# Optimization experiments

Measured on AMD Instinct MI355X. Metric: run time of the kernel, lower is better.

Reference implementation:

```python
import jax, jax.numpy as jnp
import numpy as np

NEG_SLOPE = 0.2  # PyG GATConv default leaky_relu slope


def gat_conv(x, src, dst, num_nodes, W, att_src, att_dst, bias, heads, out_ch, concat):
    """PyG-style GATConv (eval mode, self-loops already included in src/dst).
    x: [N, in_ch]; src/dst: [E] int; W: [in_ch, heads*out_ch];
    att_src/att_dst: [heads, out_ch]; bias: [heads*out_ch] or [out_ch].
    """
    N = num_nodes
    h = (x @ W).reshape(N, heads, out_ch)                      # [N, H, C]
    a_src = jnp.einsum('nhc,hc->nh', h, att_src)               # [N, H]
    a_dst = jnp.einsum('nhc,hc->nh', h, att_dst)               # [N, H]
    e = jax.nn.leaky_relu(a_src[src] + a_dst[dst], NEG_SLOPE)  # [E, H]
    # segment softmax over incoming edges of each dst node
    m = jax.ops.segment_max(e, dst, num_segments=N)            # [N, H]
    m = jnp.where(jnp.isfinite(m), m, 0.0)
    w = jnp.exp(e - m[dst])                                    # [E, H]
    denom = jax.ops.segment_sum(w, dst, num_segments=N)        # [N, H]
    alpha = w / denom[dst]                                     # [E, H]
    msg = alpha[:, :, None] * h[src]                           # [E, H, C]
    out = jax.ops.segment_sum(msg, dst, num_segments=N)        # [N, H, C]
    if concat:
        out = out.reshape(N, heads * out_ch)
    else:
        out = out.mean(axis=1)
    return out + bias


def setup_inputs() -> dict:
    key = jax.random.key(0)
    ks = jax.random.split(key, 10)
    N, E, in_ch, hidden, heads = 50000, 800000, 128, 64, 4
    x = jax.random.normal(ks[0], (N, in_ch), dtype=jnp.float32)
    edge_index = jax.random.randint(ks[1], (2, E), 0, N, dtype=jnp.int64)
    s1 = float(np.sqrt(1.0 / in_ch))
    W1 = jax.random.normal(ks[2], (in_ch, heads * hidden), dtype=jnp.float32) * s1
    att_src1 = jax.random.normal(ks[3], (heads, hidden), dtype=jnp.float32) * 0.1
    att_dst1 = jax.random.normal(ks[4], (heads, hidden), dtype=jnp.float32) * 0.1
    bias1 = jnp.zeros((heads * hidden,), dtype=jnp.float32)
    s2 = float(np.sqrt(1.0 / (heads * hidden)))
    W2 = jax.random.normal(ks[5], (heads * hidden, 1), dtype=jnp.float32) * s2
    att_src2 = jax.random.normal(ks[6], (1, 1), dtype=jnp.float32) * 0.1
    att_dst2 = jax.random.normal(ks[7], (1, 1), dtype=jnp.float32) * 0.1
    bias2 = jnp.zeros((1,), dtype=jnp.float32)
    return {"x": x, "edge_index": edge_index, "W1": W1, "att_src1": att_src1,
            "att_dst1": att_dst1, "bias1": bias1, "W2": W2, "att_src2": att_src2,
            "att_dst2": att_dst2, "bias2": bias2}


def reference(x, edge_index, W1, att_src1, att_dst1, bias1, W2, att_src2, att_dst2, bias2):
    N = x.shape[0]
    hidden, heads = 64, 4
    loops = jnp.arange(N, dtype=edge_index.dtype)
    src = jnp.concatenate([edge_index[0], loops])  # PyG adds self-loops
    dst = jnp.concatenate([edge_index[1], loops])
    # eval mode -> dropout is identity
    h = gat_conv(x, src, dst, N, W1, att_src1, att_dst1, bias1, heads, hidden, True)
    h = jax.nn.elu(h)
    out = gat_conv(h, src, dst, N, W2, att_src2, att_dst2, bias2, 1, 1, False)
    return out.squeeze(-1)  # [N]
```

## Files before the change

### kernel.cpp

```cpp
#include <hip/hip_runtime.h>
#include <hip/hip_fp16.h>
#include <math.h>

#define INC 128
#define F1 256
#define HEADS 4
#define NEG_SLOPE 0.2f

typedef _Float16 f16x8 __attribute__((ext_vector_type(8)));
typedef float f32x4 __attribute__((ext_vector_type(4)));

__global__ __launch_bounds__(256) void prep_kernel(
    const float* __restrict__ W1, _Float16* __restrict__ W1T,
    const float* __restrict__ att_s, const float* __restrict__ att_d,
    float* __restrict__ w1s, float* __restrict__ w1d,
    const int* __restrict__ ei, int* __restrict__ deg, int* __restrict__ rank,
    int E, int Etot, int nw1t)
{
    int b = blockIdx.x;
    if (b < nw1t) {
        int i = b * 256 + threadIdx.x;
        int k = i >> 8;
        int c = i & 255;
        W1T[c * 128 + k] = (_Float16)W1[i];
    } else if (b < nw1t + ((Etot + 255) >> 8)) {
        int e = (b - nw1t) * 256 + threadIdx.x;
        if (e < Etot) {
            int d = (e < E) ? ei[E + e] : (e - E);
            rank[e] = atomicAdd(&deg[d], 1);
        }
    } else {
        #pragma unroll
        for (int rep = 0; rep < 2; ++rep) {
            int idx = threadIdx.x + rep * 256;
            int h = idx >> 7;
            int k = idx & 127;
            float ss = 0.f, sd = 0.f;
            for (int c = 0; c < 64; ++c) {
                float w = W1[k * F1 + h * 64 + c];
                ss += w * att_s[h * 64 + c];
                sd += w * att_d[h * 64 + c];
            }
            w1s[h * 128 + k] = ss;
            w1d[h * 128 + k] = sd;
        }
    }
}

__global__ __launch_bounds__(256) void scan1_kernel(
    const int* __restrict__ deg, int* __restrict__ incl,
    int* __restrict__ bsum, int N)
{
    __shared__ int tmp[256];
    int i = blockIdx.x * 256 + threadIdx.x;
    int v = (i < N) ? deg[i] : 0;
    tmp[threadIdx.x] = v;
    __syncthreads();
    for (int o = 1; o < 256; o <<= 1) {
        int add = (threadIdx.x >= o) ? tmp[threadIdx.x - o] : 0;
        __syncthreads();
        tmp[threadIdx.x] += add;
        __syncthreads();
    }
    if (i < N) incl[i] = tmp[threadIdx.x];
    if (threadIdx.x == 255) bsum[blockIdx.x] = tmp[255];
}

__global__ __launch_bounds__(256) void scan3_kernel(
    const int* __restrict__ deg, const int* __restrict__ incl,
    const int* __restrict__ bsum, int* __restrict__ off,
    int N, int Etot, int nb)
{
    __shared__ int tmp[256];
    const int bid = blockIdx.x;
    const int t = threadIdx.x;
    tmp[t] = (t < bid && t < nb) ? bsum[t] : 0;
    __syncthreads();
    #pragma unroll
    for (int o = 128; o > 0; o >>= 1) {
        if (t < o) tmp[t] += tmp[t + o];
        __syncthreads();
    }
    int pre = tmp[0];
    int i = bid * 256 + t;
    if (i < N) {
        off[i] = incl[i] - deg[i] + pre;
    } else if (i == N) {
        off[N] = Etot;
    }
}

__global__ __launch_bounds__(256) void mid_kernel(
    const int* __restrict__ ei, const int* __restrict__ rank,
    const int* __restrict__ off, int* __restrict__ esrc,
    const float* __restrict__ x, const float* __restrict__ w1s,
    const float* __restrict__ w1d, float* __restrict__ a_src,
    float* __restrict__ a_dst, unsigned* __restrict__ x_h,
    int N, int E, int Etot, int egrid)
{
    if ((int)blockIdx.x < egrid) {
        int e = blockIdx.x * 256 + threadIdx.x;
        if (e < Etot) {
            int s, d;
            if (e < E) { s = ei[e]; d = ei[E + e]; }
            else       { s = d = e - E; }
            esrc[off[d] + rank[e]] = s;
        }
        return;
    }
    int wave = threadIdx.x >> 6;
    int lane = threadIdx.x & 63;
    int n = (blockIdx.x - egrid) * 4 + wave;
    if (n >= N) return;
    float2 xv = *(const float2*)&x[(size_t)n * INC + lane * 2];
    __half2 xh = __floats2half2_rn(xv.x, xv.y);
    x_h[(size_t)n * 64 + lane] = *(unsigned*)&xh;
    float ps[4], pd[4];
    #pragma unroll
    for (int h = 0; h < 4; ++h) {
        float2 ws = *(const float2*)&w1s[h * 128 + lane * 2];
        float2 wd = *(const float2*)&w1d[h * 128 + lane * 2];
        ps[h] = xv.x * ws.x + xv.y * ws.y;
        pd[h] = xv.x * wd.x + xv.y * wd.y;
    }
    #pragma unroll
    for (int o = 32; o > 0; o >>= 1) {
        #pragma unroll
        for (int h = 0; h < 4; ++h) {
            ps[h] += __shfl_xor(ps[h], o);
            pd[h] += __shfl_xor(pd[h], o);
        }
    }
    if (lane == 0) {
        *(float4*)&a_src[n * HEADS] = make_float4(ps[0], ps[1], ps[2], ps[3]);
        *(float4*)&a_dst[n * HEADS] = make_float4(pd[0], pd[1], pd[2], pd[3]);
    }
}

__global__ __launch_bounds__(256) void aggx_kernel(
    const unsigned* __restrict__ x_h, const float* __restrict__ a_src,
    const float* __restrict__ a_dst, const int* __restrict__ off,
    const int* __restrict__ esrc, __half* __restrict__ agg, int N)
{
    __shared__ unsigned lalh[4][64][4];
    __shared__ int lsrc_s[4][64];

    const int wave = threadIdx.x >> 6;
    const int lane = threadIdx.x & 63;
    const int n = blockIdx.x * 4 + wave;
    if (n >= N) return;

    const int beg = off[n], end = off[n + 1];
    const int deg = end - beg;
    const float4* a_src4 = (const float4*)a_src;
    float4 ad4 = *(const float4*)&a_dst[n * HEADS];
    float ad[4] = {ad4.x, ad4.y, ad4.z, ad4.w};

    __half2 acc[4];
    #pragma unroll
    for (int h = 0; h < 4; ++h) acc[h] = __float2half2_rn(0.f);

    #define GATHER(CNT)                                                          \
    {                                                                            \
        int j = 0;                                                               \
        for (; j + 4 <= (CNT); j += 4) {                                         \
            int s0 = lsrc_s[wave][j + 0];                                        \
            int s1 = lsrc_s[wave][j + 1];                                        \
            int s2 = lsrc_s[wave][j + 2];                                        \
            int s3 = lsrc_s[wave][j + 3];                                        \
            unsigned v0 = x_h[(size_t)s0 * 64 + lane];                           \
            unsigned v1 = x_h[(size_t)s1 * 64 + lane];                           \
            unsigned v2 = x_h[(size_t)s2 * 64 + lane];                           \
            unsigned v3 = x_h[(size_t)s3 * 64 + lane];                           \
            uint4 a0 = *(uint4*)&lalh[wave][j + 0][0];                           \
            uint4 a1 = *(uint4*)&lalh[wave][j + 1][0];                           \
            uint4 a2 = *(uint4*)&lalh[wave][j + 2][0];                           \
            uint4 a3 = *(uint4*)&lalh[wave][j + 3][0];                           \
            __half2 h0 = *(__half2*)&v0, h1v = *(__half2*)&v1;                   \
            __half2 h2v = *(__half2*)&v2, h3 = *(__half2*)&v3;                   \
            acc[0] = __hfma2(*(__half2*)&a0.x, h0, acc[0]);                      \
            acc[1] = __hfma2(*(__half2*)&a0.y, h0, acc[1]);                      \
            acc[2] = __hfma2(*(__half2*)&a0.z, h0, acc[2]);                      \
            acc[3] = __hfma2(*(__half2*)&a0.w, h0, acc[3]);                      \
            acc[0] = __hfma2(*(__half2*)&a1.x, h1v, acc[0]);                     \
            acc[1] = __hfma2(*(__half2*)&a1.y, h1v, acc[1]);                     \
            acc[2] = __hfma2(*(__half2*)&a1.z, h1v, acc[2]);                     \
            acc[3] = __hfma2(*(__half2*)&a1.w, h1v, acc[3]);                     \
            acc[0] = __hfma2(*(__half2*)&a2.x, h2v, acc[0]);                     \
            acc[1] = __hfma2(*(__half2*)&a2.y, h2v, acc[1]);                     \
            acc[2] = __hfma2(*(__half2*)&a2.z, h2v, acc[2]);                     \
            acc[3] = __hfma2(*(__half2*)&a2.w, h2v, acc[3]);                     \
            acc[0] = __hfma2(*(__half2*)&a3.x, h3, acc[0]);                      \
            acc[1] = __hfma2(*(__half2*)&a3.y, h3, acc[1]);                      \
            acc[2] = __hfma2(*(__half2*)&a3.z, h3, acc[2]);                      \
            acc[3] = __hfma2(*(__half2*)&a3.w, h3, acc[3]);                      \
        }                                                                        \
        for (; j < (CNT); ++j) {                                                 \
            int s0 = lsrc_s[wave][j];                                            \
            unsigned v0 = x_h[(size_t)s0 * 64 + lane];                           \
            uint4 a0 = *(uint4*)&lalh[wave][j][0];                               \
            __half2 h0 = *(__half2*)&v0;                                         \
            acc[0] = __hfma2(*(__half2*)&a0.x, h0, acc[0]);                      \
            acc[1] = __hfma2(*(__half2*)&a0.y, h0, acc[1]);                      \
            acc[2] = __hfma2(*(__half2*)&a0.z, h0, acc[2]);                      \
            acc[3] = __hfma2(*(__half2*)&a0.w, h0, acc[3]);                      \
        }                                                                        \
    }

    if (deg <= 64) {
        int i = beg + lane;
        bool valid = i < end;
        int sN = esrc[valid ? i : beg];
        float4 a4 = a_src4[sN];
        float av[4] = {a4.x, a4.y, a4.z, a4.w};
        float ev[4];
        #pragma unroll
        for (int h = 0; h < 4; ++h) {
            float e = av[h] + ad[h];
            e = e > 0.f ? e : NEG_SLOPE * e;
            ev[h] = valid ? e : -1e30f;
        }
        float m[4] = {ev[0], ev[1], ev[2], ev[3]};
        #pragma unroll
        for (int o = 32; o > 0; o >>= 1) {
            #pragma unroll
            for (int h = 0; h < 4; ++h) m[h] = fmaxf(m[h], __shfl_xor(m[h], o));
        }
        float at[4];
        #pragma unroll
        for (int h = 0; h < 4; ++h) at[h] = valid ? __expf(ev[h] - m[h]) : 0.f;
        float s[4] = {at[0], at[1], at[2], at[3]};
        #pragma unroll
        for (int o = 32; o > 0; o >>= 1) {
            #pragma unroll
            for (int h = 0; h < 4; ++h) s[h] += __shfl_xor(s[h], o);
        }
        uint4 pack;
        __half2 t0 = __float2half2_rn(at[0] / s[0]);
        __half2 t1 = __float2half2_rn(at[1] / s[1]);
        __half2 t2 = __float2half2_rn(at[2] / s[2]);
        __half2 t3 = __float2half2_rn(at[3] / s[3]);
        pack.x = *(unsigned*)&t0; pack.y = *(unsigned*)&t1;
        pack.z = *(unsigned*)&t2; pack.w = *(unsigned*)&t3;
        *(uint4*)&lalh[wave][lane][0] = pack;
        lsrc_s[wave][lane] = sN;

        GATHER(deg);
    } else {
        float m[4] = {-1e30f, -1e30f, -1e30f, -1e30f};
        float s[4] = {0.f, 0.f, 0.f, 0.f};
        for (int i = beg + lane; i < end; i += 64) {
            int sN = esrc[i];
            float4 a4 = a_src4[sN];
            float av[4] = {a4.x, a4.y, a4.z, a4.w};
            #pragma unroll
            for (int h = 0; h < 4; ++h) {
                float e = av[h] + ad[h];
                e = e > 0.f ? e : NEG_SLOPE * e;
                float nm = fmaxf(m[h], e);
                s[h] = s[h] * __expf(m[h] - nm) + __expf(e - nm);
                m[h] = nm;
            }
        }
        #pragma unroll
        for (int o = 32; o > 0; o >>= 1) {
            #pragma unroll
            for (int h = 0; h < 4; ++h) {
                float om = __shfl_xor(m[h], o);
                float os = __shfl_xor(s[h], o);
                float nm = fmaxf(m[h], om);
                s[h] = s[h] * __expf(m[h] - nm) + os * __expf(om - nm);
                m[h] = nm;
            }
        }
        float inv[4];
        #pragma unroll
        for (int h = 0; h < 4; ++h) inv[h] = 1.f / s[h];

        for (int c0 = beg; c0 < end; c0 += 64) {
            int i = c0 + lane;
            if (i < end) {
                int sN = esrc[i];
                float4 a4 = a_src4[sN];
                float av[4] = {a4.x, a4.y, a4.z, a4.w};
                uint4 pack;
                #pragma unroll
                for (int h = 0; h < 4; ++h) {
                    float e = av[h] + ad[h];
                    e = e > 0.f ? e : NEG_SLOPE * e;
                    __half2 a2h = __float2half2_rn(__expf(e - m[h]) * inv[h]);
                    ((unsigned*)&pack)[h] = *(unsigned*)&a2h;
                }
                *(uint4*)&lalh[wave][lane][0] = pack;
                lsrc_s[wave][lane] = sN;
            }
            int cend = end - c0;
            if (cend > 64) cend = 64;
            GATHER(cend);
        }
    }
    #undef GATHER

    #pragma unroll
    for (int h = 0; h < 4; ++h)
        *(unsigned*)&agg[(size_t)n * 512 + h * 128 + lane * 2] = *(unsigned*)&acc[h];
}

__global__ __launch_bounds__(256, 4) void gemm2_kernel(
    const __half* __restrict__ agg, const _Float16* __restrict__ W1T,
    const float* __restrict__ bias1, const float* __restrict__ W2,
    float* __restrict__ z, int N)
{
    __shared__ __align__(16) _Float16 stg[32 * 520];
    __shared__ float zpart[2][32];

    const int tid = threadIdx.x;
    const int w = tid >> 6;
    const int lane = tid & 63;
    const int q = lane >> 4;
    const int c16 = lane & 15;
    const int row0 = blockIdx.x * 32;
    const int rg = w & 1;
    const int cg = w >> 1;

    #pragma unroll
    for (int it = 0; it < 8; ++it) {
        int flat = (tid + it * 256) * 8;
        int r = flat >> 9;
        int c = flat & 511;
        int row = row0 + r;
        uint4 v = (row < N) ? *(const uint4*)&agg[(size_t)row * 512 + c]
                            : make_uint4(0, 0, 0, 0);
        *(uint4*)&stg[r * 520 + c] = v;
    }
    __syncthreads();

    const int row_l = rg * 16 + c16;
    f16x8 af[2][4];
    #pragma unroll
    for (int hh = 0; hh < 2; ++hh) {
        int h = cg * 2 + hh;
        #pragma unroll
        for (int kc = 0; kc < 4; ++kc)
            af[hh][kc] = *(const f16x8*)&stg[row_l * 520 + h * 128 + kc * 32 + q * 8];
    }

    float pz[4] = {};
    #pragma unroll
    for (int hh = 0; hh < 2; ++hh) {
        #pragma unroll
        for (int t = 0; t < 4; ++t) {
            int col = cg * 128 + hh * 64 + t * 16 + c16;
            f32x4 acc = {0.f, 0.f, 0.f, 0.f};
            #pragma unroll
            for (int kc = 0; kc < 4; ++kc) {
                f16x8 b = *(const f16x8*)&W1T[(size_t)col * 128 + kc * 32 + q * 8];
                acc = __builtin_amdgcn_mfma_f32_16x16x32_f16(af[hh][kc], b, acc, 0, 0, 0);
            }
            float bv = bias1[col];
            float wv = W2[col];
            #pragma unroll
            for (int reg = 0; reg < 4; ++reg) {
                float o = acc[reg] + bv;
                o = o > 0.f ? o : __expf(o) - 1.f;
                pz[reg] = fmaf(o, wv, pz[reg]);
            }
        }
    }

    #pragma unroll
    for (int o = 8; o > 0; o >>= 1) {
        #pragma unroll
        for (int reg = 0; reg < 4; ++reg) pz[reg] += __shfl_xor(pz[reg], o);
    }
    if (c16 == 0) {
        #pragma unroll
        for (int reg = 0; reg < 4; ++reg)
            zpart[cg][rg * 16 + q * 4 + reg] = pz[reg];
    }
    __syncthreads();
    if (tid < 32) {
        int row = row0 + tid;
        if (row < N) z[row] = zpart[0][tid] + zpart[1][tid];
    }
}

__global__ __launch_bounds__(256) void agg2_kernel(
    const float* __restrict__ z, const int* __restrict__ off,
    const int* __restrict__ esrc, const float* __restrict__ att_s2,
    const float* __restrict__ att_d2, const float* __restrict__ bias2,
    float* __restrict__ out, int N)
{
    int wave = threadIdx.x >> 6;
    int lane = threadIdx.x & 63;
    int n = blockIdx.x * 4 + wave;
    if (n >= N) return;
    float as2 = att_s2[0], ad2 = att_d2[0];
    int beg = off[n], end = off[n + 1];
    int deg = end - beg;
    float dstterm = z[n] * ad2;

    if (deg <= 64) {
        int i = beg + lane;
        bool valid = i < end;
        int sN = esrc[valid ? i : beg];
        float zv = z[sN];
        float e = zv * as2 + dstterm;
        e = e > 0.f ? e : NEG_SLOPE * e;
        float ev = valid ? e : -1e30f;
        float m = ev;
        #pragma unroll
        for (int o = 32; o > 0; o >>= 1) m = fmaxf(m, __shfl_xor(m, o));
        float at = valid ? __expf(ev - m) : 0.f;
        float s = at, wv = at * zv;
        #pragma unroll
        for (int o = 32; o > 0; o >>= 1) {
            s += __shfl_xor(s, o);
            wv += __shfl_xor(wv, o);
        }
        if (lane == 0) out[n] = wv / s + bias2[0];
    } else {
        float m = -1e30f, s = 0.f, wv = 0.f;
        for (int i = beg + lane; i < end; i += 64) {
            int sN = esrc[i];
            float zv = z[sN];
            float e = zv * as2 + dstterm;
            e = e > 0.f ? e : NEG_SLOPE * e;
            float nm = fmaxf(m, e);
            float c0 = __expf(m - nm), c1 = __expf(e - nm);
            s = s * c0 + c1;
            wv = wv * c0 + c1 * zv;
            m = nm;
        }
        #pragma unroll
        for (int o = 32; o > 0; o >>= 1) {
            float om = __shfl_xor(m, o), os = __shfl_xor(s, o), ow = __shfl_xor(wv, o);
            float nm = fmaxf(m, om);
            float c0 = __expf(m - nm), c1 = __expf(om - nm);
            s = s * c0 + os * c1;
            wv = wv * c0 + ow * c1;
            m = nm;
        }
        if (lane == 0) out[n] = wv / s + bias2[0];
    }
}

extern "C" void kernel_launch(void* const* d_in, const int* in_sizes, int n_in,
                              void* d_out, int out_size, void* d_ws, size_t ws_size,
                              hipStream_t stream)
{
    const float* x        = (const float*)d_in[0];
    const int*   ei       = (const int*)d_in[1];
    const float* W1       = (const float*)d_in[2];
    const float* att_src1 = (const float*)d_in[3];
    const float* att_dst1 = (const float*)d_in[4];
    const float* bias1    = (const float*)d_in[5];
    const float* W2       = (const float*)d_in[6];
    const float* att_src2 = (const float*)d_in[7];
    const float* att_dst2 = (const float*)d_in[8];
    const float* bias2    = (const float*)d_in[9];
    float* out = (float*)d_out;

    int N = in_sizes[0] / INC;
    int E = in_sizes[1] / 2;
    int Etot = E + N;

    char* p = (char*)d_ws;
    auto alloc = [&](size_t bytes) {
        void* r = (void*)p;
        p += (bytes + 255) & ~(size_t)255;
        return r;
    };
    unsigned* x_h   = (unsigned*)alloc((size_t)N * 64 * 4);
    __half* agg     = (__half*)alloc((size_t)N * 512 * 2);
    _Float16* W1T   = (_Float16*)alloc((size_t)INC * F1 * 2);
    float* w1s    = (float*)alloc(4 * 128 * 4);
    float* w1d    = (float*)alloc(4 * 128 * 4);
    float* a_src1 = (float*)alloc((size_t)N * HEADS * 4);
    float* a_dst1 = (float*)alloc((size_t)N * HEADS * 4);
    float* z      = (float*)alloc((size_t)N * 4);
    int* deg    = (int*)alloc((size_t)N * 4);
    int* incl   = (int*)alloc((size_t)N * 4);
    int* off    = (int*)alloc((size_t)(N + 1) * 4);
    int* rank   = (int*)alloc((size_t)Etot * 4);
    int* bsum   = (int*)alloc(1024);
    int* esrc   = (int*)alloc((size_t)Etot * 4);

    hipMemsetAsync(deg, 0, (size_t)N * 4, stream);

    int nw1t = INC * F1 / 256;
    int egrid = (Etot + 255) / 256;
    prep_kernel<<<nw1t + egrid + 1, 256, 0, stream>>>(
        W1, W1T, att_src1, att_dst1, w1s, w1d, ei, deg, rank, E, Etot, nw1t);

    int nb = (N + 255) / 256;
    scan1_kernel<<<nb, 256, 0, stream>>>(deg, incl, bsum, N);

    int nb1 = (N + 1 + 255) / 256;
    scan3_kernel<<<nb1, 256, 0, stream>>>(deg, incl, bsum, off, N, Etot, nb);

    int nlog = (N + 3) / 4;
    mid_kernel<<<egrid + nlog, 256, 0, stream>>>(
        ei, rank, off, esrc, x, w1s, w1d, a_src1, a_dst1, x_h, N, E, Etot, egrid);

    int ngrid1 = (N + 3) / 4;
    aggx_kernel<<<ngrid1, 256, 0, stream>>>(x_h, a_src1, a_dst1, off, esrc, agg, N);

    int ng2 = (N + 31) / 32;
    gemm2_kernel<<<ng2, 256, 0, stream>>>(agg, W1T, bias1, W2, z, N);

    int ngrid2 = (N + 3) / 4;
    agg2_kernel<<<ngrid2, 256, 0, stream>>>(z, off, esrc, att_src2, att_dst2, bias2, out, N);
}
```

Measured before the change: 181.5 us.

## Fuse layer-1 aggregation with the second GEMM and ELU projection

The layer-1 aggregation kernel now stages its per-node fp16 aggregated features in shared memory, then runs the W1 MFMA product, bias, ELU and the dot product with W2 in the same block to produce z directly. This removes the separate gemm2 kernel and the round trip of the N×512 fp16 intermediate through global memory. In exchange each 4-node block re-reads all of W1T from cache, uses only 4 of 16 MFMA rows, and adds block-wide barriers that tie together waves whose nodes have uneven degrees.

```diff
diff --git a/kernel.cpp b/kernel.cpp
--- a/kernel.cpp
+++ b/kernel.cpp
@@ -9,6 +9,12 @@
 
 typedef _Float16 f16x8 __attribute__((ext_vector_type(8)));
 typedef float f32x4 __attribute__((ext_vector_type(4)));
+
+static __device__ __forceinline__ f16x8 f16x8_zero() {
+    f16x8 v = {(_Float16)0, (_Float16)0, (_Float16)0, (_Float16)0,
+               (_Float16)0, (_Float16)0, (_Float16)0, (_Float16)0};
+    return v;
+}
 
 __global__ __launch_bounds__(256) void prep_kernel(
     const float* __restrict__ W1, _Float16* __restrict__ W1T,
@@ -140,21 +146,29 @@
 __global__ __launch_bounds__(256) void aggx_kernel(
     const unsigned* __restrict__ x_h, const float* __restrict__ a_src,
     const float* __restrict__ a_dst, const int* __restrict__ off,
-    const int* __restrict__ esrc, __half* __restrict__ agg, int N)
+    const int* __restrict__ esrc, const _Float16* __restrict__ W1T,
+    const float* __restrict__ bias1, const float* __restrict__ W2,
+    float* __restrict__ z, int N)
 {
     __shared__ unsigned lalh[4][64][4];
     __shared__ int lsrc_s[4][64];
+    __shared__ __align__(16) _Float16 aggl[4][4][144];
+    __shared__ float zpart[4][4];
 
     const int wave = threadIdx.x >> 6;
     const int lane = threadIdx.x & 63;
     const int n = blockIdx.x * 4 + wave;
-    if (n >= N) return;
-
-    const int beg = off[n], end = off[n + 1];
+    const bool nvalid = n < N;
+
+    int beg = 0, end = 0;
+    if (nvalid) { beg = off[n]; end = off[n + 1]; }
     const int deg = end - beg;
     const float4* a_src4 = (const float4*)a_src;
-    float4 ad4 = *(const float4*)&a_dst[n * HEADS];
-    float ad[4] = {ad4.x, ad4.y, ad4.z, ad4.w};
+    float ad[4] = {0.f, 0.f, 0.f, 0.f};
+    if (nvalid) {
+        float4 ad4 = *(const float4*)&a_dst[n * HEADS];
+        ad[0] = ad4.x; ad[1] = ad4.y; ad[2] = ad4.z; ad[3] = ad4.w;
+    }
 
     __half2 acc[4];
     #pragma unroll
@@ -207,7 +221,7 @@
         }                                                                        \
     }
 
-    if (deg <= 64) {
+    if (deg > 0 && deg <= 64) {
         int i = beg + lane;
         bool valid = i < end;
         int sN = esrc[valid ? i : beg];
@@ -246,7 +260,7 @@
         lsrc_s[wave][lane] = sN;
 
         GATHER(deg);
-    } else {
+    } else if (deg > 64) {
         float m[4] = {-1e30f, -1e30f, -1e30f, -1e30f};
         float s[4] = {0.f, 0.f, 0.f, 0.f};
         for (int i = beg + lane; i < end; i += 64) {
@@ -303,85 +317,51 @@
 
     #pragma unroll
     for (int h = 0; h < 4; ++h)
-        *(unsigned*)&agg[(size_t)n * 512 + h * 128 + lane * 2] = *(unsigned*)&acc[h];
-}
-
-__global__ __launch_bounds__(256, 4) void gemm2_kernel(
-    const __half* __restrict__ agg, const _Float16* __restrict__ W1T,
-    const float* __restrict__ bias1, const float* __restrict__ W2,
-    float* __restrict__ z, int N)
-{
-    __shared__ __align__(16) _Float16 stg[32 * 520];
-    __shared__ float zpart[2][32];
-
-    const int tid = threadIdx.x;
-    const int w = tid >> 6;
-    const int lane = tid & 63;
+        *(unsigned*)&aggl[h][wave][lane * 2] = *(unsigned*)&acc[h];
+    __syncthreads();
+
     const int q = lane >> 4;
     const int c16 = lane & 15;
-    const int row0 = blockIdx.x * 32;
-    const int rg = w & 1;
-    const int cg = w >> 1;
-
-    #pragma unroll
-    for (int it = 0; it < 8; ++it) {
-        int flat = (tid + it * 256) * 8;
-        int r = flat >> 9;
-        int c = flat & 511;
-        int row = row0 + r;
-        uint4 v = (row < N) ? *(const uint4*)&agg[(size_t)row * 512 + c]
-                            : make_uint4(0, 0, 0, 0);
-        *(uint4*)&stg[r * 520 + c] = v;
+    f16x8 af[4];
+    #pragma unroll
+    for (int kc = 0; kc < 4; ++kc) {
+        af[kc] = (c16 < 4) ? *(const f16x8*)&aggl[wave][c16][kc * 32 + q * 8]
+                           : f16x8_zero();
+    }
+    float pz[4] = {};
+    #pragma unroll
+    for (int t = 0; t < 4; ++t) {
+        int col = wave * 64 + t * 16 + c16;
+        f32x4 dacc = {0.f, 0.f, 0.f, 0.f};
+        #pragma unroll
+        for (int kc = 0; kc < 4; ++kc) {
+            f16x8 b = *(const f16x8*)&W1T[(size_t)col * 128 + kc * 32 + q * 8];
+            dacc = __builtin_amdgcn_mfma_f32_16x16x32_f16(af[kc], b, dacc, 0, 0, 0);
+        }
+        float bv = bias1[col];
+        float wv = W2[col];
+        #pragma unroll
+        for (int reg = 0; reg < 4; ++reg) {
+            float o = dacc[reg] + bv;
+            o = o > 0.f ? o : __expf(o) - 1.f;
+            pz[reg] = fmaf(o, wv, pz[reg]);
+        }
+    }
+    #pragma unroll
+    for (int o = 8; o > 0; o >>= 1) {
+        #pragma unroll
+        for (int reg = 0; reg < 4; ++reg) pz[reg] += __shfl_xor(pz[reg], o);
+    }
+    if (lane == 0) {
+        #pragma unroll
+        for (int reg = 0; reg < 4; ++reg) zpart[wave][reg] = pz[reg];
     }
     __syncthreads();
-
-    const int row_l = rg * 16 + c16;
-    f16x8 af[2][4];
-    #pragma unroll
-    for (int hh = 0; hh < 2; ++hh) {
-        int h = cg * 2 + hh;
-        #pragma unroll
-        for (int kc = 0; kc < 4; ++kc)
-            af[hh][kc] = *(const f16x8*)&stg[row_l * 520 + h * 128 + kc * 32 + q * 8];
-    }
-
-    float pz[4] = {};
-    #pragma unroll
-    for (int hh = 0; hh < 2; ++hh) {
-        #pragma unroll
-        for (int t = 0; t < 4; ++t) {
-            int col = cg * 128 + hh * 64 + t * 16 + c16;
-            f32x4 acc = {0.f, 0.f, 0.f, 0.f};
-            #pragma unroll
-            for (int kc = 0; kc < 4; ++kc) {
-                f16x8 b = *(const f16x8*)&W1T[(size_t)col * 128 + kc * 32 + q * 8];
-                acc = __builtin_amdgcn_mfma_f32_16x16x32_f16(af[hh][kc], b, acc, 0, 0, 0);
-            }
-            float bv = bias1[col];
-            float wv = W2[col];
-            #pragma unroll
-            for (int reg = 0; reg < 4; ++reg) {
-                float o = acc[reg] + bv;
-                o = o > 0.f ? o : __expf(o) - 1.f;
-                pz[reg] = fmaf(o, wv, pz[reg]);
-            }
-        }
-    }
-
-    #pragma unroll
-    for (int o = 8; o > 0; o >>= 1) {
-        #pragma unroll
-        for (int reg = 0; reg < 4; ++reg) pz[reg] += __shfl_xor(pz[reg], o);
-    }
-    if (c16 == 0) {
-        #pragma unroll
-        for (int reg = 0; reg < 4; ++reg)
-            zpart[cg][rg * 16 + q * 4 + reg] = pz[reg];
-    }
-    __syncthreads();
-    if (tid < 32) {
-        int row = row0 + tid;
-        if (row < N) z[row] = zpart[0][tid] + zpart[1][tid];
+    if (threadIdx.x < 4) {
+        int row = blockIdx.x * 4 + threadIdx.x;
+        if (row < N)
+            z[row] = zpart[0][threadIdx.x] + zpart[1][threadIdx.x] +
+                     zpart[2][threadIdx.x] + zpart[3][threadIdx.x];
     }
 }
 
@@ -472,7 +452,6 @@
         return r;
     };
     unsigned* x_h   = (unsigned*)alloc((size_t)N * 64 * 4);
-    __half* agg     = (__half*)alloc((size_t)N * 512 * 2);
     _Float16* W1T   = (_Float16*)alloc((size_t)INC * F1 * 2);
     float* w1s    = (float*)alloc(4 * 128 * 4);
     float* w1d    = (float*)alloc(4 * 128 * 4);
@@ -504,10 +483,8 @@
         ei, rank, off, esrc, x, w1s, w1d, a_src1, a_dst1, x_h, N, E, Etot, egrid);
 
     int ngrid1 = (N + 3) / 4;
-    aggx_kernel<<<ngrid1, 256, 0, stream>>>(x_h, a_src1, a_dst1, off, esrc, agg, N);
-
-    int ng2 = (N + 31) / 32;
-    gemm2_kernel<<<ng2, 256, 0, stream>>>(agg, W1T, bias1, W2, z, N);
+    aggx_kernel<<<ngrid1, 256, 0, stream>>>(
+        x_h, a_src1, a_dst1, off, esrc, W1T, bias1, W2, z, N);
 
     int ngrid2 = (N + 3) / 4;
     agg2_kernel<<<ngrid2, 256, 0, stream>>>(z, off, esrc, att_src2, att_dst2, bias2, out, N);
```

After: 232.6 us. 28.2% more time.
